# Performance work log

Measured on AMD Instinct MI355X. Metric: run time of the kernel, lower is better.

## Reference

```python
import jax, jax.numpy as jnp
import numpy as np

N, E, D_IN, D_H, D_OUT, W = 100000, 1600000, 128, 128, 128, 3
HTC_W, TEMP = 0.01, 1.0  # curvature c = 1.0


def _project(x):
    n = jnp.maximum(jnp.linalg.norm(x, axis=-1, keepdims=True), 1e-12)
    return x * jnp.minimum((1.0 - 1e-5) / n, 1.0)


def _artanh(x):
    x = jnp.clip(x, -1.0 + 1e-6, 1.0 - 1e-6)
    return 0.5 * (jnp.log1p(x) - jnp.log1p(-x))


def _expmap0(v):
    n = jnp.maximum(jnp.linalg.norm(v, axis=-1, keepdims=True), 1e-12)
    return _project(jnp.tanh(n) * v / n)


def _logmap0(y):
    y = _project(y)
    n = jnp.maximum(jnp.linalg.norm(y, axis=-1, keepdims=True), 1e-12)
    return _artanh(n) * y / n


def setup_inputs() -> dict:
    key = jax.random.key(0)
    ks = jax.random.split(key, 24)
    x = jax.random.normal(ks[0], (N, D_IN), dtype=jnp.float32)
    edge_index = jax.random.randint(ks[1], (2, E), 0, N)
    t = jax.random.uniform(ks[2], (E,), dtype=jnp.float32)
    prev_hyp = _project(jax.random.normal(ks[3], (N, D_OUT), dtype=jnp.float32) * 0.05)
    lengths = jax.random.randint(ks[4], (N,), 0, W + 1)
    valid_mask = jnp.arange(W)[None, :] < lengths[:, None]  # front-filled deque
    hist_hyp = _project(jax.random.normal(ks[5], (N, W, D_OUT), dtype=jnp.float32) * 0.05)
    hist_hyp = hist_hyp * valid_mask[..., None].astype(jnp.float32)  # padded slots are zero

    def lin(k, dout, din):
        return jax.random.normal(k, (dout, din), dtype=jnp.float32) / np.sqrt(din)

    params = dict(
        w_time=jax.random.normal(ks[6], (D_IN,), dtype=jnp.float32),
        b_time=jnp.zeros((D_IN,), jnp.float32),
        W0_l=lin(ks[7], D_H, D_IN), b0_l=jnp.zeros((D_H,), jnp.float32), W0_r=lin(ks[8], D_H, D_IN),
        W1_l=lin(ks[9], D_OUT, D_H), b1_l=jnp.zeros((D_OUT,), jnp.float32), W1_r=lin(ks[10], D_OUT, D_H),
        W_ih=lin(ks[11], 3 * D_OUT, D_OUT), W_hh=lin(ks[12], 3 * D_OUT, D_OUT),
        b_ih=jnp.zeros((3 * D_OUT,), jnp.float32), b_hh=jnp.zeros((3 * D_OUT,), jnp.float32),
        Wq=lin(ks[13], D_OUT, D_OUT), Wk=lin(ks[14], D_OUT, D_OUT), Wv=lin(ks[15], D_OUT, D_OUT),
    )
    return dict(x=x, edge_index=edge_index, t=t, prev_hyp=prev_hyp,
                hist_hyp=hist_hyp, valid_mask=valid_mask, **params)


def reference(x, edge_index, t, prev_hyp, hist_hyp, valid_mask,
              w_time, b_time, W0_l, b0_l, W0_r, W1_l, b1_l, W1_r,
              W_ih, W_hh, b_ih, b_hh, Wq, Wk, Wv):
    n = x.shape[0]
    src, dst = edge_index[0], edge_index[1]
    ones_e = jnp.ones_like(t)
    # per-node mean event time over incident edges (src and dst both count)
    nt = jax.ops.segment_sum(t, src, n) + jax.ops.segment_sum(t, dst, n)
    cnt = jax.ops.segment_sum(ones_e, src, n) + jax.ops.segment_sum(ones_e, dst, n)
    node_time = nt / jnp.maximum(cnt, 1.0)
    x = x + jnp.cos(node_time[:, None] * w_time[None, :] + b_time[None, :])
    # SAGEConv (mean aggr over incoming edges): out = W_l @ mean_j x_j + b + W_r @ x_i
    deg = jnp.maximum(jax.ops.segment_sum(ones_e, dst, n), 1.0)[:, None]
    agg0 = jax.ops.segment_sum(x[src], dst, n) / deg
    h = jax.nn.relu(agg0 @ W0_l.T + b0_l + x @ W0_r.T)
    agg1 = jax.ops.segment_sum(h[src], dst, n) / deg
    h_now = agg1 @ W1_l.T + b1_l + h @ W1_r.T  # tangent-space current embedding

    prev_tan = _logmap0(prev_hyp)
    # ragged history attention (padded + masked)
    hist_tan = _logmap0(hist_hyp)                       # [N, W, D]
    q = h_now @ Wq.T                                    # [N, D]
    k = hist_tan @ Wk.T                                 # [N, W, D]
    v = hist_tan @ Wv.T
    score = jnp.einsum('nwd,nd->nw', k, q) / (np.sqrt(D_OUT) * max(TEMP, 1e-6))
    has_hist = valid_mask.any(axis=-1, keepdims=True)
    score = jnp.where(valid_mask, score, -jnp.inf)
    score = jnp.where(has_hist, score, 0.0)
    alpha = jax.nn.softmax(score, axis=-1)
    alpha = jnp.where(has_hist, alpha, 0.0)
    ctx = jnp.einsum('nw,nwd->nd', alpha, v)

    # GRUCell(input=h_now, hidden=prev_tan + ctx)
    hidden = prev_tan + ctx
    gi = h_now @ W_ih.T + b_ih
    gh = hidden @ W_hh.T + b_hh
    i_r, i_z, i_n = jnp.split(gi, 3, axis=-1)
    h_r, h_z, h_n = jnp.split(gh, 3, axis=-1)
    r = jax.nn.sigmoid(i_r + h_r)
    z = jax.nn.sigmoid(i_z + h_z)
    nn_ = jnp.tanh(i_n + r * h_n)
    h_tan = (1.0 - z) * nn_ + z * hidden
    h_hyp = _expmap0(h_tan)

    # hyperbolic temporal consistency aux loss (c = 1)
    x_sq = jnp.sum(h_hyp * h_hyp, axis=-1)
    y_sq = jnp.sum(prev_hyp * prev_hyp, axis=-1)
    diff_sq = jnp.sum((h_hyp - prev_hyp) ** 2, axis=-1)
    denom = jnp.maximum((1.0 - x_sq) * (1.0 - y_sq), 1e-8)
    zarg = jnp.maximum(1.0 + 2.0 * diff_sq / denom, 1.0 + 1e-6)
    dist = jnp.arccosh(zarg)
    valid_prev = (jnp.sum(jnp.abs(prev_hyp), axis=-1) > 0).astype(dist.dtype)
    aux = HTC_W * jnp.sum(dist * valid_prev) / jnp.maximum(jnp.sum(valid_prev), 1.0)
    aux = jnp.where(jnp.any(valid_prev > 0), aux, 0.0)
    return h_hyp, aux
```

## Files before the change

### kernel.cpp

```cpp
#include <hip/hip_runtime.h>
#include <math.h>


typedef _Float16 f16x8 __attribute__((ext_vector_type(8)));
typedef _Float16 f16x4 __attribute__((ext_vector_type(4)));
typedef _Float16 f16x2 __attribute__((ext_vector_type(2)));
typedef float f32x4 __attribute__((ext_vector_type(4)));

__device__ __forceinline__ float wsum(float v) {
#pragma unroll
  for (int off = 1; off < 64; off <<= 1) v += __shfl_xor(v, off, 64);
  return v;
}

__device__ __forceinline__ void fsplit(float x, _Float16& h, _Float16& l) {
  h = (_Float16)x;
  l = (_Float16)(x - (float)h);
}

__device__ __forceinline__ float logmap_scale(float nrm2) {
  float n0 = fmaxf(sqrtf(nrm2), 1e-12f);
  float sp = fminf((1.0f - 1e-5f) / n0, 1.0f);
  float np = fmaxf(n0 * sp, 1e-12f);
  float a  = fminf(np, 1.0f - 1e-6f);
  float at = 0.5f * (log1pf(a) - log1pf(-a));
  return sp * at / np;
}

__global__ void k_edge(const int* __restrict__ ei, const float* __restrict__ t,
                       unsigned long long* __restrict__ packed, int E) {
  int e = blockIdx.x * 256 + threadIdx.x;
  if (e >= E) return;
  int s = ei[e], d = ei[E + e];
  unsigned long long tf =
      (unsigned long long)__float2uint_rn(t[e] * 16777216.0f);
  unsigned long long encs = tf | (1ULL << 40);
  atomicAdd(&packed[s], encs);
  atomicAdd(&packed[d], encs | (1ULL << 52));
}

__global__ void k_scan1(const unsigned long long* __restrict__ packed,
                        int* __restrict__ rowptr, int* __restrict__ bsum, int N) {
  __shared__ int s[256];
  int t = threadIdx.x;
  int base = blockIdx.x * 1024 + t * 4;
  int v[4]; int loc = 0;
#pragma unroll
  for (int j = 0; j < 4; ++j) {
    int i = base + j;
    v[j] = (i < N) ? (int)(packed[i] >> 52) : 0;
    loc += v[j];
  }
  s[t] = loc; __syncthreads();
  for (int off = 1; off < 256; off <<= 1) {
    int x = (t >= off) ? s[t - off] : 0; __syncthreads();
    s[t] += x; __syncthreads();
  }
  int run = s[t] - loc;
#pragma unroll
  for (int j = 0; j < 4; ++j) { int i = base + j; if (i < N) rowptr[i] = run; run += v[j]; }
  if (t == 255) bsum[blockIdx.x] = s[255];
}

__global__ void k_scan2(const int* __restrict__ bsum, int* __restrict__ boff, int nb) {
  __shared__ int s[128];
  int t = threadIdx.x;
  int v = (t < nb) ? bsum[t] : 0;
  s[t] = v; __syncthreads();
  for (int off = 1; off < 128; off <<= 1) {
    int x = (t >= off) ? s[t - off] : 0; __syncthreads();
    s[t] += x; __syncthreads();
  }
  boff[t] = s[t] - v;
}

__global__ void k_scan3(int* __restrict__ rowptr, const int* __restrict__ boff, int N, int E) {
  int i = blockIdx.x * 256 + threadIdx.x;
  if (i < N) rowptr[i] += boff[i >> 10];
  if (i == 0) rowptr[N] = E;
}

__global__ void k_scatter(const int* __restrict__ ei, const int* __restrict__ rowptr,
                          int* __restrict__ cursor, int* __restrict__ eidx, int E) {
  int e = blockIdx.x * 256 + threadIdx.x;
  if (e >= E) return;
  int s = ei[e], d = ei[E + e];
  int p = rowptr[d] + atomicAdd(&cursor[d], 1);
  eidx[p] = s;
}

__global__ void k_time(const float* __restrict__ x,
                       const unsigned long long* __restrict__ packed,
                       const float* __restrict__ wt,
                       const float* __restrict__ bt, float* __restrict__ outF,
                       _Float16* __restrict__ outH, _Float16* __restrict__ outL, int N) {
  int id = blockIdx.x * 256 + threadIdx.x;
  if (id >= N * 32) return;
  int n = id >> 5, q = id & 31;
  unsigned long long p = packed[n];
  float tsum = (float)(p & 0xFFFFFFFFFFULL) * 5.9604644775390625e-8f;
  int c = (int)((p >> 40) & 0xFFF);
  float tm = tsum / fmaxf((float)c, 1.0f);
  float4 xv = ((const float4*)x)[id];
  float4 wv = ((const float4*)wt)[q];
  float4 bv = ((const float4*)bt)[q];
  float o[4];
  o[0] = xv.x + cosf(tm * wv.x + bv.x);
  o[1] = xv.y + cosf(tm * wv.y + bv.y);
  o[2] = xv.z + cosf(tm * wv.z + bv.z);
  o[3] = xv.w + cosf(tm * wv.w + bv.w);
  ((float4*)outF)[id] = make_float4(o[0], o[1], o[2], o[3]);
  f16x4 vh, vl;
#pragma unroll
  for (int j = 0; j < 4; ++j) { _Float16 h, l; fsplit(o[j], h, l); vh[j] = h; vl[j] = l; }
  *(f16x4*)&outH[(size_t)id * 4] = vh;
  *(f16x4*)&outL[(size_t)id * 4] = vl;
}

__global__ void k_agg(const float* __restrict__ X, const int* __restrict__ rowptr,
                      const int* __restrict__ eidx, _Float16* __restrict__ outH,
                      _Float16* __restrict__ outL, int N) {
  int wid = threadIdx.x >> 6, lane = threadIdx.x & 63;
  int n = blockIdx.x * 4 + wid;
  if (n >= N) return;
  int s0 = rowptr[n], s1 = rowptr[n + 1];
  float ax = 0.f, ay = 0.f;
  for (int e = s0; e < s1; ++e) {
    int s = eidx[e];
    float2 v = ((const float2*)X)[(size_t)s * 64 + lane];
    ax += v.x; ay += v.y;
  }
  float sc = 1.0f / fmaxf((float)(s1 - s0), 1.0f);
  _Float16 hx, lx, hy, ly;
  fsplit(ax * sc, hx, lx); fsplit(ay * sc, hy, ly);
  f16x2 vh = {hx, hy}, vl = {lx, ly};
  *(f16x2*)&outH[(size_t)n * 128 + lane * 2] = vh;
  *(f16x2*)&outL[(size_t)n * 128 + lane * 2] = vl;
}

__global__ void k_prep(const float* __restrict__ W0l, const float* __restrict__ W0r,
                       const float* __restrict__ W1l, const float* __restrict__ W1r,
                       const float* __restrict__ Wv,  const float* __restrict__ Wih,
                       const float* __restrict__ Whh, const float* __restrict__ bih,
                       const float* __restrict__ bhh,
                       _Float16* __restrict__ W0H, _Float16* __restrict__ W0L,
                       _Float16* __restrict__ W1H, _Float16* __restrict__ W1L,
                       _Float16* __restrict__ WvH, _Float16* __restrict__ WvL,
                       _Float16* __restrict__ WzH, _Float16* __restrict__ WzL,
                       float* __restrict__ bz) {
  int id = blockIdx.x * 256 + threadIdx.x;
  if (id < 32768) {
    int c = id >> 8, k = id & 255;
    float v0 = (k < 128) ? W0l[c * 128 + k] : W0r[c * 128 + (k - 128)];
    float v1 = (k < 128) ? W1l[c * 128 + k] : W1r[c * 128 + (k - 128)];
    fsplit(v0, W0H[id], W0L[id]);
    fsplit(v1, W1H[id], W1L[id]);
  }
  if (id < 16384) {
    fsplit(Wv[id], WvH[id], WvL[id]);
  }
  if (id < 131072) {
    int c = id >> 8, k = id & 255;
    float v;
    if (c < 256)      v = (k < 128) ? Wih[c * 128 + k] : Whh[c * 128 + (k - 128)];
    else if (c < 384) v = (k < 128) ? Wih[c * 128 + k] : 0.f;
    else              v = (k < 128) ? 0.f : Whh[(c - 128) * 128 + (k - 128)];
    fsplit(v, WzH[id], WzL[id]);
  }
  if (id < 512) {
    float v;
    if (id < 256)      v = bih[id] + bhh[id];
    else if (id < 384) v = bih[id];
    else               v = bhh[id - 128];
    bz[id] = v;
  }
}

__global__ void k_ct(const float* __restrict__ Wk, const float* __restrict__ Wq,
                     _Float16* __restrict__ CtH, _Float16* __restrict__ CtL) {
  int id = blockIdx.x * 256 + threadIdx.x;
  if (id >= 16384) return;
  int c = id >> 7, k = id & 127;
  float s = 0.f;
  for (int j = 0; j < 128; ++j) s += Wk[j * 128 + c] * Wq[j * 128 + k];
  fsplit(s, CtH[id], CtL[id]);
}

__global__ __launch_bounds__(256)
void k_mm(const _Float16* __restrict__ A1H, const _Float16* __restrict__ A1L,
          const _Float16* __restrict__ A2H, const _Float16* __restrict__ A2L,
          const _Float16* __restrict__ WH,  const _Float16* __restrict__ WL,
          const float* __restrict__ bias,   const float* __restrict__ addb,
          float* __restrict__ outF, _Float16* __restrict__ outH,
          _Float16* __restrict__ outL,
          int Nrows, int Ktot, int Ctot, int relu) {
  __shared__ _Float16 sA[2][128][64];
  __shared__ _Float16 sW[2][128][64];
  const int tid = threadIdx.x;
  const int lane = tid & 63;
  const int wv = tid >> 6;
  const int wr = wv >> 1, wc = wv & 1;
  const int laneR = lane & 15, laneG = lane >> 4;
  const int n0 = blockIdx.x * 128;
  const int c0 = blockIdx.y * 128;

  f32x4 acc[4][4];
#pragma unroll
  for (int mi = 0; mi < 4; ++mi)
#pragma unroll
    for (int ni = 0; ni < 4; ++ni)
#pragma unroll
      for (int j = 0; j < 4; ++j) acc[mi][ni][j] = 0.f;

  const int nslab = Ktot >> 6;
  for (int s = 0; s < nslab; ++s) {
    int kglob = s << 6;
    const _Float16* aH = (kglob < 128) ? A1H : A2H;
    const _Float16* aL = (kglob < 128) ? A1L : A2L;
    int kc = kglob & 127;
    __syncthreads();
#pragma unroll
    for (int it = 0; it < 4; ++it) {
      int idx = tid + (it << 8);
      int r = idx >> 3, chunk = idx & 7;
      int cs = (chunk ^ (r & 7)) << 3;
      int kq = chunk << 3;
      int n = n0 + r;
      f16x8 vh, vl;
      if (n < Nrows) {
        vh = *(const f16x8*)&aH[(size_t)n * 128 + kc + kq];
        vl = *(const f16x8*)&aL[(size_t)n * 128 + kc + kq];
      } else {
#pragma unroll
        for (int j = 0; j < 8; ++j) { vh[j] = (_Float16)0; vl[j] = (_Float16)0; }
      }
      *(f16x8*)&sA[0][r][cs] = vh;
      *(f16x8*)&sA[1][r][cs] = vl;
      int c = c0 + r;
      f16x8 wh = *(const f16x8*)&WH[(size_t)c * Ktot + kglob + kq];
      f16x8 wl = *(const f16x8*)&WL[(size_t)c * Ktot + kglob + kq];
      *(f16x8*)&sW[0][r][cs] = wh;
      *(f16x8*)&sW[1][r][cs] = wl;
    }
    __syncthreads();
#pragma unroll
    for (int kk = 0; kk < 2; ++kk) {
      f16x8 ah[4], al[4], bh[4], bl[4];
      int kch = (kk << 2) + laneG;
#pragma unroll
      for (int m = 0; m < 4; ++m) {
        int row = wr * 64 + m * 16 + laneR;
        int ko = (kch ^ (row & 7)) << 3;
        ah[m] = *(const f16x8*)&sA[0][row][ko];
        al[m] = *(const f16x8*)&sA[1][row][ko];
      }
#pragma unroll
      for (int n = 0; n < 4; ++n) {
        int row = wc * 64 + n * 16 + laneR;
        int ko = (kch ^ (row & 7)) << 3;
        bh[n] = *(const f16x8*)&sW[0][row][ko];
        bl[n] = *(const f16x8*)&sW[1][row][ko];
      }
#pragma unroll
      for (int m = 0; m < 4; ++m)
#pragma unroll
        for (int n = 0; n < 4; ++n) {
          acc[m][n] = __builtin_amdgcn_mfma_f32_16x16x32_f16(ah[m], bh[n], acc[m][n], 0, 0, 0);
          acc[m][n] = __builtin_amdgcn_mfma_f32_16x16x32_f16(al[m], bh[n], acc[m][n], 0, 0, 0);
          acc[m][n] = __builtin_amdgcn_mfma_f32_16x16x32_f16(ah[m], bl[n], acc[m][n], 0, 0, 0);
        }
    }
  }
#pragma unroll
  for (int m = 0; m < 4; ++m) {
#pragma unroll
    for (int n = 0; n < 4; ++n) {
      int rbase = n0 + wr * 64 + m * 16 + laneG * 4;
      int c = c0 + wc * 64 + n * 16 + laneR;
      float bval = bias ? bias[c] : 0.f;
#pragma unroll
      for (int j = 0; j < 4; ++j) {
        int r = rbase + j;
        if (r >= Nrows) continue;
        float v = acc[m][n][j] + bval;
        if (addb) v += addb[(size_t)r * Ctot + c];
        if (relu) v = fmaxf(v, 0.f);
        if (outF) outF[(size_t)r * Ctot + c] = v;
        if (outH) {
          _Float16 h, l; fsplit(v, h, l);
          outH[(size_t)r * Ctot + c] = h;
          outL[(size_t)r * Ctot + c] = l;
        }
      }
    }
  }
}

__global__ __launch_bounds__(512, 4)
void k_gru(const _Float16* __restrict__ P0H, const _Float16* __restrict__ P0L,
           const _Float16* __restrict__ P2H, const _Float16* __restrict__ P2L,
           const _Float16* __restrict__ WzH, const _Float16* __restrict__ WzL,
           const float* __restrict__ bz, const float* __restrict__ prev,
           float* __restrict__ out, float* __restrict__ pd,
           float* __restrict__ pv, int N) {
  __shared__ _Float16 sA[2][128][64];
  __shared__ _Float16 sW[2][128][64];
  __shared__ float rn1[128][2];
  __shared__ float rn3[128][2][3];
  __shared__ float distrow[128], validrow[128];
  __shared__ float sred[2][2];
  const int tid = threadIdx.x;
  const int lane = tid & 63;
  const int wv = tid >> 6;
  const int wr = wv >> 1, wc = wv & 1;
  const int laneR = lane & 15, laneG = lane >> 4;
  const int n0 = blockIdx.x * 128;

  f32x4 acc[4][2][4];
#pragma unroll
  for (int q = 0; q < 4; ++q)
#pragma unroll
    for (int m = 0; m < 2; ++m)
#pragma unroll
      for (int n = 0; n < 4; ++n)
#pragma unroll
        for (int j = 0; j < 4; ++j) acc[q][m][n][j] = 0.f;

#define STAGE_W(Q)                                                          \
  {                                                                         \
    _Pragma("unroll")                                                       \
    for (int it = 0; it < 2; ++it) {                                        \
      int idx = tid + (it << 9);                                            \
      int r = idx >> 3, chunk = idx & 7;                                    \
      int cs = (chunk ^ (r & 7)) << 3;                                      \
      int kq = chunk << 3;                                                  \
      size_t wrow = (size_t)((Q)*128 + r);                                  \
      *(f16x8*)&sW[0][r][cs] = *(const f16x8*)&WzH[wrow * 256 + kglob + kq];\
      *(f16x8*)&sW[1][r][cs] = *(const f16x8*)&WzL[wrow * 256 + kglob + kq];\
    }                                                                       \
  }

#define COMPUTE_Q(Q)                                                        \
  {                                                                         \
    _Pragma("unroll")                                                       \
    for (int kk = 0; kk < 2; ++kk) {                                        \
      int kch = (kk << 2) + laneG;                                          \
      f16x8 ah[2], al[2], bh[4], bl[4];                                     \
      _Pragma("unroll")                                                     \
      for (int m = 0; m < 2; ++m) {                                         \
        int row = wr * 32 + m * 16 + laneR;                                 \
        int ko = (kch ^ (row & 7)) << 3;                                    \
        ah[m] = *(const f16x8*)&sA[0][row][ko];                             \
        al[m] = *(const f16x8*)&sA[1][row][ko];                             \
      }                                                                     \
      _Pragma("unroll")                                                     \
      for (int n = 0; n < 4; ++n) {                                         \
        int row = wc * 64 + n * 16 + laneR;                                 \
        int ko = (kch ^ (row & 7)) << 3;                                    \
        bh[n] = *(const f16x8*)&sW[0][row][ko];                             \
        bl[n] = *(const f16x8*)&sW[1][row][ko];                             \
      }                                                                     \
      _Pragma("unroll")                                                     \
      for (int m = 0; m < 2; ++m)                                           \
        _Pragma("unroll")                                                   \
        for (int n = 0; n < 4; ++n) {                                       \
          acc[Q][m][n] = __builtin_amdgcn_mfma_f32_16x16x32_f16(ah[m], bh[n], acc[Q][m][n], 0, 0, 0); \
          acc[Q][m][n] = __builtin_amdgcn_mfma_f32_16x16x32_f16(al[m], bh[n], acc[Q][m][n], 0, 0, 0); \
          acc[Q][m][n] = __builtin_amdgcn_mfma_f32_16x16x32_f16(ah[m], bl[n], acc[Q][m][n], 0, 0, 0); \
        }                                                                   \
    }                                                                       \
  }

#pragma unroll
  for (int s = 0; s < 4; ++s) {
    int kglob = s << 6;
    const _Float16* aH = (s < 2) ? P0H : P2H;
    const _Float16* aL = (s < 2) ? P0L : P2L;
    int kc = kglob & 127;
    __syncthreads();
#pragma unroll
    for (int it = 0; it < 2; ++it) {
      int idx = tid + (it << 9);
      int r = idx >> 3, chunk = idx & 7;
      int cs = (chunk ^ (r & 7)) << 3;
      int kq = chunk << 3;
      int n = n0 + r;
      f16x8 vh, vl;
      if (n < N) {
        vh = *(const f16x8*)&aH[(size_t)n * 128 + kc + kq];
        vl = *(const f16x8*)&aL[(size_t)n * 128 + kc + kq];
      } else {
#pragma unroll
        for (int j = 0; j < 8; ++j) { vh[j] = (_Float16)0; vl[j] = (_Float16)0; }
      }
      *(f16x8*)&sA[0][r][cs] = vh;
      *(f16x8*)&sA[1][r][cs] = vl;
    }
    STAGE_W(0);
    __syncthreads();
    COMPUTE_Q(0);
    __syncthreads();
    STAGE_W(1);
    __syncthreads();
    COMPUTE_Q(1);
    __syncthreads();
    if (s < 2) {
      STAGE_W(2);
      __syncthreads();
      COMPUTE_Q(2);
    } else {
      STAGE_W(3);
      __syncthreads();
      COMPUTE_Q(3);
    }
  }
#undef STAGE_W
#undef COMPUTE_Q

  float bz0[4], bz1[4], bz2[4], bz3[4];
#pragma unroll
  for (int n = 0; n < 4; ++n) {
    int d = wc * 64 + n * 16 + laneR;
    bz0[n] = bz[d]; bz1[n] = bz[128 + d]; bz2[n] = bz[256 + d]; bz3[n] = bz[384 + d];
  }
  float tv[2][4][4];
#pragma unroll
  for (int m = 0; m < 2; ++m)
#pragma unroll
    for (int n = 0; n < 4; ++n)
#pragma unroll
      for (int j = 0; j < 4; ++j) {
        int row = n0 + wr * 32 + m * 16 + laneG * 4 + j;
        int d = wc * 64 + n * 16 + laneR;
        float hid = 0.f;
        if (row < N) {
          size_t o = (size_t)row * 128 + d;
          hid = (float)P2H[o] + (float)P2L[o];
        }
        float gr = acc[0][m][n][j] + bz0[n];
        float gz = acc[1][m][n][j] + bz1[n];
        float gi = acc[2][m][n][j] + bz2[n];
        float gh = acc[3][m][n][j] + bz3[n];
        float rr = 1.f / (1.f + expf(-gr));
        float zz = 1.f / (1.f + expf(-gz));
        float nn = tanhf(gi + rr * gh);
        tv[m][n][j] = (1.f - zz) * nn + zz * hid;
      }
#pragma unroll
  for (int m = 0; m < 2; ++m)
#pragma unroll
    for (int j = 0; j < 4; ++j) {
      float p = 0.f;
#pragma unroll
      for (int n = 0; n < 4; ++n) p += tv[m][n][j] * tv[m][n][j];
#pragma unroll
      for (int off = 1; off < 16; off <<= 1) p += __shfl_xor(p, off, 64);
      if (laneR == 0) rn1[wr * 32 + m * 16 + laneG * 4 + j][wc] = p;
    }
  __syncthreads();
  float hv[2][4][4];
#pragma unroll
  for (int m = 0; m < 2; ++m)
#pragma unroll
    for (int j = 0; j < 4; ++j) {
      int rl = wr * 32 + m * 16 + laneG * 4 + j;
      int row = n0 + rl;
      float nv2 = rn1[rl][0] + rn1[rl][1];
      float nv = fmaxf(sqrtf(nv2), 1e-12f);
      float tn = tanhf(nv);
      float s1 = tn / nv;
      float nw = fmaxf(tn, 1e-12f);
      float sp = fminf((1.f - 1e-5f) / nw, 1.f);
      float scl = s1 * sp;
#pragma unroll
      for (int n = 0; n < 4; ++n) {
        float h = tv[m][n][j] * scl;
        hv[m][n][j] = h;
        int d = wc * 64 + n * 16 + laneR;
        if (row < N) out[(size_t)row * 128 + d] = h;
      }
    }
#pragma unroll
  for (int m = 0; m < 2; ++m)
#pragma unroll
    for (int j = 0; j < 4; ++j) {
      int rl = wr * 32 + m * 16 + laneG * 4 + j;
      int row = n0 + rl;
      float ys = 0.f, ds = 0.f, pa = 0.f;
#pragma unroll
      for (int n = 0; n < 4; ++n) {
        int d = wc * 64 + n * 16 + laneR;
        float p = (row < N) ? prev[(size_t)row * 128 + d] : 0.f;
        float h = hv[m][n][j];
        ys += p * p; ds += (h - p) * (h - p); pa += fabsf(p);
      }
#pragma unroll
      for (int off = 1; off < 16; off <<= 1) {
        ys += __shfl_xor(ys, off, 64);
        ds += __shfl_xor(ds, off, 64);
        pa += __shfl_xor(pa, off, 64);
      }
      if (laneR == 0) { rn3[rl][wc][0] = ys; rn3[rl][wc][1] = ds; rn3[rl][wc][2] = pa; }
    }
  __syncthreads();
  if (wc == 0 && laneR == 0) {
#pragma unroll
    for (int m = 0; m < 2; ++m)
#pragma unroll
      for (int j = 0; j < 4; ++j) {
        int rl = wr * 32 + m * 16 + laneG * 4 + j;
        int row = n0 + rl;
        float nv2 = rn1[rl][0] + rn1[rl][1];
        float nv = fmaxf(sqrtf(nv2), 1e-12f);
        float tn = tanhf(nv);
        float s1 = tn / nv;
        float nw = fmaxf(tn, 1e-12f);
        float sp = fminf((1.f - 1e-5f) / nw, 1.f);
        float scl = s1 * sp;
        float x_sq = scl * scl * nv2;
        float y_sq = rn3[rl][0][0] + rn3[rl][1][0];
        float d_sq = rn3[rl][0][1] + rn3[rl][1][1];
        float pab  = rn3[rl][0][2] + rn3[rl][1][2];
        float denom = fmaxf((1.f - x_sq) * (1.f - y_sq), 1e-8f);
        float zarg = fmaxf(1.f + 2.f * d_sq / denom, 1.f + 1e-6f);
        float dist = acoshf(zarg);
        float valid = (pab > 0.f && row < N) ? 1.f : 0.f;
        distrow[rl] = dist * valid;
        validrow[rl] = valid;
      }
  }
  __syncthreads();
  if (tid < 128) {
    float dv = distrow[tid], vvv = validrow[tid];
    dv = wsum(dv); vvv = wsum(vvv);
    if ((tid & 63) == 0) { sred[tid >> 6][0] = dv; sred[tid >> 6][1] = vvv; }
  }
  __syncthreads();
  if (tid == 0) {
    pd[blockIdx.x] = sred[0][0] + sred[1][0];
    pv[blockIdx.x] = sred[0][1] + sred[1][1];
  }
}

__global__ void k_logmap(const float* __restrict__ Y, float* __restrict__ out, int N) {
  int wid = threadIdx.x >> 6, lane = threadIdx.x & 63;
  int n = blockIdx.x * 4 + wid;
  if (n >= N) return;
  float2 y = ((const float2*)Y)[(size_t)n * 64 + lane];
  float nrm2 = wsum(y.x * y.x + y.y * y.y);
  float s = logmap_scale(nrm2);
  ((float2*)out)[(size_t)n * 64 + lane] = make_float2(y.x * s, y.y * s);
}

__global__ void k_attn(const float* __restrict__ U, const float* __restrict__ hist,
                       _Float16* __restrict__ outH, _Float16* __restrict__ outL, int N) {
  int wid = threadIdx.x >> 6, lane = threadIdx.x & 63;
  int n = blockIdx.x * 4 + wid;
  if (n >= N) return;
  float2 u = ((const float2*)U)[(size_t)n * 64 + lane];
  float htx[3], hty[3], sc[3];
  bool val[3];
#pragma unroll
  for (int w = 0; w < 3; ++w) {
    float2 h = ((const float2*)hist)[((size_t)n * 3 + w) * 64 + lane];
    float nrm2 = wsum(h.x * h.x + h.y * h.y);
    val[w] = nrm2 > 0.f;
    float s = logmap_scale(nrm2);
    htx[w] = h.x * s; hty[w] = h.y * s;
    float d = wsum(htx[w] * u.x + hty[w] * u.y);
    sc[w] = d * 0.0883883476483184f;
  }
  float cx = 0.f, cy = 0.f;
  if (val[0] || val[1] || val[2]) {
    float m = -INFINITY;
#pragma unroll
    for (int w = 0; w < 3; ++w) if (val[w]) m = fmaxf(m, sc[w]);
    float a[3]; float ssum = 0.f;
#pragma unroll
    for (int w = 0; w < 3; ++w) { a[w] = val[w] ? expf(sc[w] - m) : 0.f; ssum += a[w]; }
    float inv = 1.f / ssum;
#pragma unroll
    for (int w = 0; w < 3; ++w) { cx += htx[w] * (a[w] * inv); cy += hty[w] * (a[w] * inv); }
  }
  _Float16 hx, lx, hy, ly;
  fsplit(cx, hx, lx); fsplit(cy, hy, ly);
  f16x2 vh = {hx, hy}, vl = {lx, ly};
  *(f16x2*)&outH[(size_t)n * 128 + lane * 2] = vh;
  *(f16x2*)&outL[(size_t)n * 128 + lane * 2] = vl;
}

__global__ void k_reduce(const float* __restrict__ pd, const float* __restrict__ pv,
                         float* __restrict__ aux_out, int nparts) {
  __shared__ float sd[256], sv[256];
  float a = 0.f, b = 0.f;
  for (int i = threadIdx.x; i < nparts; i += 256) { a += pd[i]; b += pv[i]; }
  sd[threadIdx.x] = a; sv[threadIdx.x] = b; __syncthreads();
  for (int off = 128; off > 0; off >>= 1) {
    if (threadIdx.x < off) { sd[threadIdx.x] += sd[threadIdx.x + off]; sv[threadIdx.x] += sv[threadIdx.x + off]; }
    __syncthreads();
  }
  if (threadIdx.x == 0) {
    float aux = (sv[0] > 0.f) ? 0.01f * sd[0] / fmaxf(sv[0], 1.f) : 0.f;
    aux_out[0] = aux;
  }
}

extern "C" void kernel_launch(void* const* d_in, const int* in_sizes, int n_in,
                              void* d_out, int out_size, void* d_ws, size_t ws_size,
                              hipStream_t stream) {
  const float* x      = (const float*)d_in[0];
  const int*   ei     = (const int*)  d_in[1];
  const float* t      = (const float*)d_in[2];
  const float* prev   = (const float*)d_in[3];
  const float* hist   = (const float*)d_in[4];
  const float* w_time = (const float*)d_in[6];
  const float* b_time = (const float*)d_in[7];
  const float* W0l    = (const float*)d_in[8];
  const float* b0l    = (const float*)d_in[9];
  const float* W0r    = (const float*)d_in[10];
  const float* W1l    = (const float*)d_in[11];
  const float* b1l    = (const float*)d_in[12];
  const float* W1r    = (const float*)d_in[13];
  const float* Wih    = (const float*)d_in[14];
  const float* Whh    = (const float*)d_in[15];
  const float* bih    = (const float*)d_in[16];
  const float* bhh    = (const float*)d_in[17];
  const float* Wq     = (const float*)d_in[18];
  const float* Wk     = (const float*)d_in[19];
  const float* Wv     = (const float*)d_in[20];

  const int N = in_sizes[0] / 128;
  const int E = in_sizes[1] / 2;
  const int NB4 = (N + 3) / 4;
  const int NB1 = (N + 1023) / 1024;
  const int NBG = (N + 127) / 128;

  char* wbase = (char*)d_ws;
  size_t off = 0;
  auto alloc = [&](size_t bytes) -> void* {
    off = (off + 255) & ~(size_t)255;
    void* p = wbase + off; off += bytes; return p;
  };
  unsigned long long* packed = (unsigned long long*)alloc((size_t)N * 8);
  int*   cursor = (int*)  alloc((size_t)N * 4);
  size_t zero_bytes = off;
  int*   rowptr = (int*)  alloc((size_t)(N + 1) * 4);
  int*   bsum   = (int*)  alloc(512);
  int*   boff   = (int*)  alloc(512);
  int*   eidx   = (int*)  alloc((size_t)E * 4);
  _Float16* W0H = (_Float16*)alloc(32768 * 2);
  _Float16* W0L = (_Float16*)alloc(32768 * 2);
  _Float16* W1H = (_Float16*)alloc(32768 * 2);
  _Float16* W1L = (_Float16*)alloc(32768 * 2);
  _Float16* CtH = (_Float16*)alloc(16384 * 2);
  _Float16* CtL = (_Float16*)alloc(16384 * 2);
  _Float16* WvH = (_Float16*)alloc(16384 * 2);
  _Float16* WvL = (_Float16*)alloc(16384 * 2);
  _Float16* WzH = (_Float16*)alloc(131072 * 2);
  _Float16* WzL = (_Float16*)alloc(131072 * 2);
  float* bz     = (float*)alloc(512 * 4);
  float* F0 = (float*)alloc((size_t)N * 128 * 4);
  float* F1 = (float*)alloc((size_t)N * 128 * 4);
  _Float16* P0H = (_Float16*)alloc((size_t)N * 128 * 2);
  _Float16* P0L = (_Float16*)alloc((size_t)N * 128 * 2);
  _Float16* P1H = (_Float16*)alloc((size_t)N * 128 * 2);
  _Float16* P1L = (_Float16*)alloc((size_t)N * 128 * 2);
  _Float16* P2H = (_Float16*)alloc((size_t)N * 128 * 2);
  _Float16* P2L = (_Float16*)alloc((size_t)N * 128 * 2);
  float* pd = (float*)alloc((size_t)NBG * 4);
  float* pv = (float*)alloc((size_t)NBG * 4);
  (void)ws_size; (void)n_in; (void)out_size;

  float* out_h   = (float*)d_out;
  float* out_aux = out_h + (size_t)N * 128;

  hipMemsetAsync(d_ws, 0, zero_bytes, stream);

  k_prep<<<512, 256, 0, stream>>>(W0l, W0r, W1l, W1r, Wv, Wih, Whh, bih, bhh,
                                  W0H, W0L, W1H, W1L, WvH, WvL, WzH, WzL, bz);
  k_ct<<<64, 256, 0, stream>>>(Wk, Wq, CtH, CtL);

  int ebl = (E + 255) / 256;
  k_edge<<<ebl, 256, 0, stream>>>(ei, t, packed, E);
  k_scan1<<<NB1, 256, 0, stream>>>(packed, rowptr, bsum, N);
  k_scan2<<<1, 128, 0, stream>>>(bsum, boff, NB1);
  k_scan3<<<(N + 255) / 256, 256, 0, stream>>>(rowptr, boff, N, E);
  k_scatter<<<ebl, 256, 0, stream>>>(ei, rowptr, cursor, eidx, E);

  k_time<<<(N * 32 + 255) / 256, 256, 0, stream>>>(x, packed, w_time, b_time,
                                                   F0, P0H, P0L, N);
  k_agg<<<NB4, 256, 0, stream>>>(F0, rowptr, eidx, P1H, P1L, N);
  dim3 gb((N + 127) / 128, 1);
  k_mm<<<gb, 256, 0, stream>>>(P1H, P1L, P0H, P0L, W0H, W0L, b0l, nullptr,
                               F1, P2H, P2L, N, 256, 128, 1);
  k_agg<<<NB4, 256, 0, stream>>>(F1, rowptr, eidx, P1H, P1L, N);
  k_mm<<<gb, 256, 0, stream>>>(P1H, P1L, P2H, P2L, W1H, W1L, b1l, nullptr,
                               nullptr, P0H, P0L, N, 256, 128, 0);
  k_mm<<<gb, 256, 0, stream>>>(P0H, P0L, nullptr, nullptr, CtH, CtL, nullptr, nullptr,
                               F0, nullptr, nullptr, N, 128, 128, 0);
  k_attn<<<NB4, 256, 0, stream>>>(F0, hist, P1H, P1L, N);
  k_logmap<<<NB4, 256, 0, stream>>>(prev, F1, N);
  k_mm<<<gb, 256, 0, stream>>>(P1H, P1L, nullptr, nullptr, WvH, WvL, nullptr, F1,
                               nullptr, P2H, P2L, N, 128, 128, 0);
  k_gru<<<NBG, 512, 0, stream>>>(P0H, P0L, P2H, P2L, WzH, WzL, bz, prev,
                                 out_h, pd, pv, N);
  k_reduce<<<1, 256, 0, stream>>>(pd, pv, out_aux, NBG);
}
```

Before: 1.301 ms.

## Load GRU weight fragments directly from global memory and halve row tile

The GRU kernel stops staging the weight matrix through shared memory and instead loads each wave's B fragments straight from global memory (expected to be cached) inside the MFMA loop. This removes the weight staging stores and most barriers per K-step. The row tile shrinks from 128 to 64 with 256 threads, so shared memory drops and the grid doubles. The cost is uncoalesced, latency-exposed global loads of weights repeated per block, with less hiding from LDS reuse.

```diff
diff --git a/kernel.cpp b/kernel.cpp
--- a/kernel.cpp
+++ b/kernel.cpp
@@ -296,25 +296,23 @@
   }
 }
 
-__global__ __launch_bounds__(512, 4)
+__global__ __launch_bounds__(256, 2)
 void k_gru(const _Float16* __restrict__ P0H, const _Float16* __restrict__ P0L,
            const _Float16* __restrict__ P2H, const _Float16* __restrict__ P2L,
            const _Float16* __restrict__ WzH, const _Float16* __restrict__ WzL,
            const float* __restrict__ bz, const float* __restrict__ prev,
            float* __restrict__ out, float* __restrict__ pd,
            float* __restrict__ pv, int N) {
-  __shared__ _Float16 sA[2][128][64];
-  __shared__ _Float16 sW[2][128][64];
-  __shared__ float rn1[128][2];
-  __shared__ float rn3[128][2][3];
-  __shared__ float distrow[128], validrow[128];
-  __shared__ float sred[2][2];
+  __shared__ _Float16 sA[2][64][64];
+  __shared__ float rn1[64][2];
+  __shared__ float rn3[64][2][3];
+  __shared__ float distrow[64], validrow[64];
   const int tid = threadIdx.x;
   const int lane = tid & 63;
   const int wv = tid >> 6;
   const int wr = wv >> 1, wc = wv & 1;
   const int laneR = lane & 15, laneG = lane >> 4;
-  const int n0 = blockIdx.x * 128;
+  const int n0 = blockIdx.x * 64;
 
   f32x4 acc[4][2][4];
 #pragma unroll
@@ -325,20 +323,6 @@
       for (int n = 0; n < 4; ++n)
 #pragma unroll
         for (int j = 0; j < 4; ++j) acc[q][m][n][j] = 0.f;
-
-#define STAGE_W(Q)                                                          \
-  {                                                                         \
-    _Pragma("unroll")                                                       \
-    for (int it = 0; it < 2; ++it) {                                        \
-      int idx = tid + (it << 9);                                            \
-      int r = idx >> 3, chunk = idx & 7;                                    \
-      int cs = (chunk ^ (r & 7)) << 3;                                      \
-      int kq = chunk << 3;                                                  \
-      size_t wrow = (size_t)((Q)*128 + r);                                  \
-      *(f16x8*)&sW[0][r][cs] = *(const f16x8*)&WzH[wrow * 256 + kglob + kq];\
-      *(f16x8*)&sW[1][r][cs] = *(const f16x8*)&WzL[wrow * 256 + kglob + kq];\
-    }                                                                       \
-  }
 
 #define COMPUTE_Q(Q)                                                        \
   {                                                                         \
@@ -347,18 +331,18 @@
       int kch = (kk << 2) + laneG;                                          \
       f16x8 ah[2], al[2], bh[4], bl[4];                                     \
       _Pragma("unroll")                                                     \
+      for (int n = 0; n < 4; ++n) {                                         \
+        size_t wrow = (size_t)((Q) * 128 + wc * 64 + n * 16 + laneR);       \
+        size_t o = wrow * 256 + kglob + (kch << 3);                         \
+        bh[n] = *(const f16x8*)&WzH[o];                                     \
+        bl[n] = *(const f16x8*)&WzL[o];                                     \
+      }                                                                     \
+      _Pragma("unroll")                                                     \
       for (int m = 0; m < 2; ++m) {                                         \
         int row = wr * 32 + m * 16 + laneR;                                 \
         int ko = (kch ^ (row & 7)) << 3;                                    \
         ah[m] = *(const f16x8*)&sA[0][row][ko];                             \
         al[m] = *(const f16x8*)&sA[1][row][ko];                             \
-      }                                                                     \
-      _Pragma("unroll")                                                     \
-      for (int n = 0; n < 4; ++n) {                                         \
-        int row = wc * 64 + n * 16 + laneR;                                 \
-        int ko = (kch ^ (row & 7)) << 3;                                    \
-        bh[n] = *(const f16x8*)&sW[0][row][ko];                             \
-        bl[n] = *(const f16x8*)&sW[1][row][ko];                             \
       }                                                                     \
       _Pragma("unroll")                                                     \
       for (int m = 0; m < 2; ++m)                                           \
@@ -380,7 +364,7 @@
     __syncthreads();
 #pragma unroll
     for (int it = 0; it < 2; ++it) {
-      int idx = tid + (it << 9);
+      int idx = tid + (it << 8);
       int r = idx >> 3, chunk = idx & 7;
       int cs = (chunk ^ (r & 7)) << 3;
       int kq = chunk << 3;
@@ -396,25 +380,15 @@
       *(f16x8*)&sA[0][r][cs] = vh;
       *(f16x8*)&sA[1][r][cs] = vl;
     }
-    STAGE_W(0);
     __syncthreads();
     COMPUTE_Q(0);
-    __syncthreads();
-    STAGE_W(1);
-    __syncthreads();
     COMPUTE_Q(1);
-    __syncthreads();
     if (s < 2) {
-      STAGE_W(2);
-      __syncthreads();
       COMPUTE_Q(2);
     } else {
-      STAGE_W(3);
-      __syncthreads();
       COMPUTE_Q(3);
     }
   }
-#undef STAGE_W
 #undef COMPUTE_Q
 
   float bz0[4], bz1[4], bz2[4], bz3[4];
@@ -530,15 +504,10 @@
       }
   }
   __syncthreads();
-  if (tid < 128) {
+  if (tid < 64) {
     float dv = distrow[tid], vvv = validrow[tid];
     dv = wsum(dv); vvv = wsum(vvv);
-    if ((tid & 63) == 0) { sred[tid >> 6][0] = dv; sred[tid >> 6][1] = vvv; }
-  }
-  __syncthreads();
-  if (tid == 0) {
-    pd[blockIdx.x] = sred[0][0] + sred[1][0];
-    pv[blockIdx.x] = sred[0][1] + sred[1][1];
+    if (tid == 0) { pd[blockIdx.x] = dv; pv[blockIdx.x] = vvv; }
   }
 }
 
@@ -633,7 +602,7 @@
   const int E = in_sizes[1] / 2;
   const int NB4 = (N + 3) / 4;
   const int NB1 = (N + 1023) / 1024;
-  const int NBG = (N + 127) / 128;
+  const int NBG = (N + 63) / 64;
 
   char* wbase = (char*)d_ws;
   size_t off = 0;
@@ -702,7 +671,7 @@
   k_logmap<<<NB4, 256, 0, stream>>>(prev, F1, N);
   k_mm<<<gb, 256, 0, stream>>>(P1H, P1L, nullptr, nullptr, WvH, WvL, nullptr, F1,
                                nullptr, P2H, P2L, N, 128, 128, 0);
-  k_gru<<<NBG, 512, 0, stream>>>(P0H, P0L, P2H, P2L, WzH, WzL, bz, prev,
+  k_gru<<<NBG, 256, 0, stream>>>(P0H, P0L, P2H, P2L, WzH, WzL, bz, prev,
                                  out_h, pd, pv, N);
   k_reduce<<<1, 256, 0, stream>>>(pd, pv, out_aux, NBG);
 }
```

Result: no change. 1.315 ms (+1.1%).
